# Optimization experiments

Measured on AMD Instinct MI355X. Metric: run time of the kernel, lower is better.

The kernel has to match this reference:

```python
import jax, jax.numpy as jnp
import numpy as np
from jax import lax

LENS = 11
R = LENS // 2


def _make_kernels(lens):
    """distance_kernel: euclidean distance of each offset from the window center.
    lens_shape_mask: binary disk (circular aperture) mask inside the lens window."""
    r = lens // 2
    yy, xx = jnp.meshgrid(jnp.arange(lens) - r, jnp.arange(lens) - r, indexing='ij')
    dist = jnp.sqrt((yy * yy + xx * xx).astype(jnp.float32))
    mask = (dist <= (r + 0.5)).astype(jnp.float32)
    return dist, mask


def setup_inputs() -> dict:
    key = jax.random.key(0)
    k1, k2, k3 = jax.random.split(key, 3)
    B, H, W = 4, 1024, 1024
    rgb = jax.random.uniform(k1, (B, 3, H, W), dtype=jnp.float32)
    # relative disparity w.r.t. focal plane (signed, ~[-4, 4])
    disp = jax.random.normal(k2, (B, 1, H, W), dtype=jnp.float32) * 2.0
    x = jnp.concatenate([rgb, disp], axis=1)
    lens_effects = jax.random.uniform(k3, (4, 1), dtype=jnp.float32) * 8.0 + 1.0
    diskernel, lens_mask = _make_kernels(LENS)
    return {"x": x, "lens_effects": lens_effects, "diskernel": diskernel, "lens_mask": lens_mask}


def reference(x, lens_effects, diskernel, lens_mask):
    """Depth-dependent scatter splatting with soft occlusion, expressed as a gather.
    Each source pixel p splats its color onto neighbors within its circle of
    confusion coc(p) = |lens_effect * disp(p)|, weighted by the disk aperture
    mask and a soft edge (clip(coc - dist + 0.5, 0, 1)). Occlusion: sources in
    front of the destination (larger disparity) dominate via a sigmoid gate.
    Scatter-to-q == gather-at-q over all kernel offsets of the padded image."""
    B, C, H, W = x.shape
    disp_dst = x[:, 3:4]
    scale = lens_effects.reshape(B, 1, 1, 1)
    # replication pad (ReplicationPad2d(lens // 2))
    xpad = jnp.pad(x, ((0, 0), (0, 0), (R, R), (R, R)), mode='edge')

    dys, dxs = np.meshgrid(np.arange(LENS), np.arange(LENS), indexing='ij')
    dys = jnp.asarray(dys.reshape(-1), dtype=jnp.int32)
    dxs = jnp.asarray(dxs.reshape(-1), dtype=jnp.int32)
    dvals = diskernel.reshape(-1)
    mvals = lens_mask.reshape(-1)

    def step(carry, inputs):
        num, den = carry
        dy, dx, d, m = inputs
        src = lax.dynamic_slice(xpad, (0, 0, dy, dx), (B, C, H, W))
        src_rgb, src_disp = src[:, :3], src[:, 3:4]
        coc = jnp.abs(scale * src_disp)                    # per-source CoC radius
        w = m * jnp.clip(coc - d + 0.5, 0.0, 1.0)          # soft disk membership
        occ = jax.nn.sigmoid(4.0 * (src_disp - disp_dst))  # front occludes back
        w = w * occ
        return (num + w * src_rgb, den + w), None

    num0 = jnp.zeros((B, 3, H, W), dtype=x.dtype)
    den0 = jnp.zeros((B, 1, H, W), dtype=x.dtype)
    (num, den), _ = lax.scan(step, (num0, den0), (dys, dxs, dvals, mvals))
    return num / (den + 1e-8)
```

## Files before the change

### kernel.cpp

```cpp
#include <hip/hip_runtime.h>

#define LENSZ 11
#define RAD   5
#define TSX   64
#define TSY   16
#define WINX  (TSX + LENSZ - 1)
#define WINY  (TSY + LENSZ - 1)
#define RS_H  78
#define RS_F  78
#define NPAIR 37
#define IMG_H 1024
#define IMG_W 1024
#define HW    (IMG_H * IMG_W)

#define C4L2  (-5.770780163555854f)
#define DEADC (-3000.0f)

typedef __fp16 v2h __attribute__((ext_vector_type(2)));

__device__ __forceinline__ float dot2acc(float acc, v2h a, v2h b) {
    asm("v_dot2_f32_f16 %0, %1, %2, %0" : "+v"(acc) : "v"(a), "v"(b));
    return acc;
}

constexpr float C0V(int dy, int dx) {
    switch (dy * dy + dx * dx) {
        case 0:  return  0.5f;
        case 1:  return -0.5f;
        case 2:  return -0.914213562f;
        case 4:  return -1.5f;
        case 5:  return -1.736067977f;
        case 8:  return -2.328427125f;
        case 9:  return -2.5f;
        case 10: return -2.662277660f;
        case 13: return -3.105551275f;
        case 16: return -3.5f;
        case 17: return -3.623105626f;
        case 18: return -3.742640687f;
        case 20: return -3.972135955f;
        case 25: return -4.5f;
        case 26: return -4.599019514f;
        case 29: return -4.885164807f;
        default: return DEADC;
    }
}

__shared__ __align__(16) float  dpl[WINY * RS_F];
__shared__ __align__(8)  __fp16 rpl[WINY * RS_H];
__shared__ __align__(8)  __fp16 gpl[WINY * RS_H];
__shared__ __align__(8)  __fp16 bpl[WINY * RS_H];

template<int ADY, int XMN, int XMX>
__device__ __forceinline__ void do_row(
    int wy, int x4, float scale, const float (&G)[4], v2h one2,
    float (&nr)[4], float (&ng)[4], float (&nb)[4], float (&dn)[4])
{
    const v2h zero2 = {(__fp16)0.f, (__fp16)0.f};
    const v2h onee2 = {(__fp16)1.f, (__fp16)1.f};
#pragma unroll
    for (int kxe = (XMN & ~1); kxe <= XMX + 3; kxe += 2) {
        const int xo = x4 + kxe;
        const float2 d2 = *reinterpret_cast<const float2*>(&dpl[wy * RS_F + xo]);
        const v2h r2 = *reinterpret_cast<const v2h*>(&rpl[wy * RS_H + xo]);
        const v2h g2 = *reinterpret_cast<const v2h*>(&gpl[wy * RS_H + xo]);
        const v2h b2 = *reinterpret_cast<const v2h*>(&bpl[wy * RS_H + xo]);
        const float coca = scale * fabsf(d2.x);
        const float cocb = scale * fabsf(d2.y);
        const v2h coc2 = __builtin_amdgcn_cvt_pkrtz(coca, cocb);
        const float Ea = __builtin_amdgcn_exp2f(fminf(C4L2 * d2.x, 63.f));
        const float Eb = __builtin_amdgcn_exp2f(fminf(C4L2 * d2.y, 63.f));
#pragma unroll
        for (int j = 0; j < 4; ++j) {
            const float c0a = C0V(ADY, kxe - j - RAD);
            const float c0b = C0V(ADY, kxe + 1 - j - RAD);
            if (c0a == DEADC && c0b == DEADC) continue;
            const float fa = fmaf(Ea, G[j], 1.f);
            const float fb = fmaf(Eb, G[j], 1.f);
            const float rr = __builtin_amdgcn_rcpf(fa * fb);
            const v2h occ2 = __builtin_amdgcn_cvt_pkrtz(rr * fb, rr * fa);
            const v2h c0h = {(__fp16)c0a, (__fp16)c0b};
            v2h t = coc2 + c0h;
            t = __builtin_elementwise_max(t, zero2);
            t = __builtin_elementwise_min(t, onee2);
            const v2h wh = t * occ2;
            nr[j] = dot2acc(nr[j], wh, r2);
            ng[j] = dot2acc(ng[j], wh, g2);
            nb[j] = dot2acc(nb[j], wh, b2);
            dn[j] = dot2acc(dn[j], wh, one2);
        }
    }
}

__global__ __launch_bounds__(256, 6) void scatter_render_kernel(
    const float* __restrict__ x,
    const float* __restrict__ lens,
    float* __restrict__ out)
{
    const int b   = blockIdx.z;
    const int bx0 = blockIdx.x * TSX;
    const int by0 = blockIdx.y * TSY;
    const int tx  = threadIdx.x;
    const int ty  = threadIdx.y;
    const int tid = ty * 16 + tx;

    const float scale = lens[b];
    const float* xb = x + (size_t)b * 4 * HW;

    for (int p = tid; p < WINY * NPAIR; p += 256) {
        int wy = p / NPAIR;
        int px = (p - wy * NPAIR) * 2;
        int gy = by0 - RAD + wy;  gy = min(max(gy, 0), IMG_H - 1);
        int g0 = bx0 - RAD + px;      g0 = min(max(g0, 0), IMG_W - 1);
        int g1 = bx0 - RAD + px + 1;  g1 = min(max(g1, 0), IMG_W - 1);
        int ba = gy * IMG_W + g0;
        int bb = gy * IMG_W + g1;
        float r0 = xb[ba],          r1 = xb[bb];
        float q0 = xb[ba + HW],     q1 = xb[bb + HW];
        float s0 = xb[ba + 2 * HW], s1 = xb[bb + 2 * HW];
        float d0 = xb[ba + 3 * HW], d1 = xb[bb + 3 * HW];
        int oh = wy * RS_H + px;
        *reinterpret_cast<v2h*>(&rpl[oh]) = __builtin_amdgcn_cvt_pkrtz(r0, r1);
        *reinterpret_cast<v2h*>(&gpl[oh]) = __builtin_amdgcn_cvt_pkrtz(q0, q1);
        *reinterpret_cast<v2h*>(&bpl[oh]) = __builtin_amdgcn_cvt_pkrtz(s0, s1);
        *reinterpret_cast<float2*>(&dpl[wy * RS_F + px]) = make_float2(d0, d1);
    }
    __syncthreads();

    const int x4 = 4 * tx;
    float G[4];
#pragma unroll
    for (int j = 0; j < 4; ++j) {
        float dd = dpl[(ty + RAD) * RS_F + x4 + j + RAD];
        G[j] = __builtin_amdgcn_exp2f(fminf(-C4L2 * dd, 63.f));
    }
    v2h one2; one2.x = (__fp16)1.f; one2.y = (__fp16)1.f;

    float nr[4] = {0.f, 0.f, 0.f, 0.f};
    float ng[4] = {0.f, 0.f, 0.f, 0.f};
    float nb[4] = {0.f, 0.f, 0.f, 0.f};
    float dn[4] = {0.f, 0.f, 0.f, 0.f};

#pragma unroll 1
    for (int t = 0; t < 2; ++t)
        do_row<5, 3, 7>(ty + t * 10, x4, scale, G, one2, nr, ng, nb, dn);
#pragma unroll 1
    for (int t = 0; t < 2; ++t)
        do_row<4, 2, 8>(ty + 1 + t * 8, x4, scale, G, one2, nr, ng, nb, dn);
#pragma unroll 1
    for (int t = 0; t < 2; ++t)
        do_row<3, 1, 9>(ty + 2 + t * 6, x4, scale, G, one2, nr, ng, nb, dn);
#pragma unroll 1
    for (int t = 0; t < 2; ++t)
        do_row<2, 0, 10>(ty + 3 + t * 4, x4, scale, G, one2, nr, ng, nb, dn);
#pragma unroll 1
    for (int t = 0; t < 2; ++t)
        do_row<1, 0, 10>(ty + 4 + t * 2, x4, scale, G, one2, nr, ng, nb, dn);
    do_row<0, 0, 10>(ty + 5, x4, scale, G, one2, nr, ng, nb, dn);

    const size_t obase = (size_t)b * 3 * HW + (size_t)(by0 + ty) * IMG_W + (bx0 + x4);

    float inv[4];
#pragma unroll
    for (int j = 0; j < 4; ++j)
        inv[j] = __builtin_amdgcn_rcpf(dn[j] + 1e-8f);

    float4 o;
    o.x = nr[0] * inv[0]; o.y = nr[1] * inv[1]; o.z = nr[2] * inv[2]; o.w = nr[3] * inv[3];
    *reinterpret_cast<float4*>(&out[obase]) = o;
    o.x = ng[0] * inv[0]; o.y = ng[1] * inv[1]; o.z = ng[2] * inv[2]; o.w = ng[3] * inv[3];
    *reinterpret_cast<float4*>(&out[obase + HW]) = o;
    o.x = nb[0] * inv[0]; o.y = nb[1] * inv[1]; o.z = nb[2] * inv[2]; o.w = nb[3] * inv[3];
    *reinterpret_cast<float4*>(&out[obase + 2 * HW]) = o;
}

extern "C" void kernel_launch(void* const* d_in, const int* in_sizes, int n_in,
                              void* d_out, int out_size, void* d_ws, size_t ws_size,
                              hipStream_t stream) {
    const float* x    = (const float*)d_in[0];
    const float* lens = (const float*)d_in[1];
    float* out        = (float*)d_out;

    const int B = in_sizes[1];

    dim3 block(16, 16, 1);
    dim3 grid(IMG_W / TSX, IMG_H / TSY, B);
    scatter_render_kernel<<<grid, block, 0, stream>>>(x, lens, out);
}
```

Baseline: 113.0 us.

## Widen tile to 128 columns with 8 outputs per thread and drop exp clamps

Each thread now computes 8 horizontally adjacent output pixels instead of 4, and the block tile doubles to 128 columns. Each loaded source pair (depth, rgb, coc, exp) is then reused across more outputs, which amortizes LDS loads and per-source exp work over a wider register window. The fminf clamps before exp2 are removed, so very large disparities could now produce inf and break the rational occlusion term. Register pressure rises, so the occupancy target drops from 6 to 4 blocks per CU.

Result: faster. 108.6 us (-3.9%).

```diff
diff --git a/kernel.cpp b/kernel.cpp
--- a/kernel.cpp
+++ b/kernel.cpp
@@ -2,13 +2,12 @@
 
 #define LENSZ 11
 #define RAD   5
-#define TSX   64
+#define TSX   128
 #define TSY   16
 #define WINX  (TSX + LENSZ - 1)
 #define WINY  (TSY + LENSZ - 1)
-#define RS_H  78
-#define RS_F  78
-#define NPAIR 37
+#define RS    140
+#define NPAIR 69
 #define IMG_H 1024
 #define IMG_W 1024
 #define HW    (IMG_H * IMG_W)
@@ -45,32 +44,31 @@
     }
 }
 
-__shared__ __align__(16) float  dpl[WINY * RS_F];
-__shared__ __align__(8)  __fp16 rpl[WINY * RS_H];
-__shared__ __align__(8)  __fp16 gpl[WINY * RS_H];
-__shared__ __align__(8)  __fp16 bpl[WINY * RS_H];
+__shared__ __align__(16) float  dpl[WINY * RS];
+__shared__ __align__(8)  __fp16 rpl[WINY * RS];
+__shared__ __align__(8)  __fp16 gpl[WINY * RS];
+__shared__ __align__(8)  __fp16 bpl[WINY * RS];
 
 template<int ADY, int XMN, int XMX>
 __device__ __forceinline__ void do_row(
-    int wy, int x4, float scale, const float (&G)[4], v2h one2,
-    float (&nr)[4], float (&ng)[4], float (&nb)[4], float (&dn)[4])
+    int wy, int x8, float scale, const float (&G)[8], v2h one2,
+    float (&nr)[8], float (&ng)[8], float (&nb)[8], float (&dn)[8])
 {
     const v2h zero2 = {(__fp16)0.f, (__fp16)0.f};
     const v2h onee2 = {(__fp16)1.f, (__fp16)1.f};
 #pragma unroll
-    for (int kxe = (XMN & ~1); kxe <= XMX + 3; kxe += 2) {
-        const int xo = x4 + kxe;
-        const float2 d2 = *reinterpret_cast<const float2*>(&dpl[wy * RS_F + xo]);
-        const v2h r2 = *reinterpret_cast<const v2h*>(&rpl[wy * RS_H + xo]);
-        const v2h g2 = *reinterpret_cast<const v2h*>(&gpl[wy * RS_H + xo]);
-        const v2h b2 = *reinterpret_cast<const v2h*>(&bpl[wy * RS_H + xo]);
-        const float coca = scale * fabsf(d2.x);
-        const float cocb = scale * fabsf(d2.y);
-        const v2h coc2 = __builtin_amdgcn_cvt_pkrtz(coca, cocb);
-        const float Ea = __builtin_amdgcn_exp2f(fminf(C4L2 * d2.x, 63.f));
-        const float Eb = __builtin_amdgcn_exp2f(fminf(C4L2 * d2.y, 63.f));
+    for (int kxe = (XMN & ~1); kxe <= XMX + 7; kxe += 2) {
+        const int xo = x8 + kxe;
+        const float2 d2 = *reinterpret_cast<const float2*>(&dpl[wy * RS + xo]);
+        const v2h r2 = *reinterpret_cast<const v2h*>(&rpl[wy * RS + xo]);
+        const v2h g2 = *reinterpret_cast<const v2h*>(&gpl[wy * RS + xo]);
+        const v2h b2 = *reinterpret_cast<const v2h*>(&bpl[wy * RS + xo]);
+        const v2h coc2 = __builtin_amdgcn_cvt_pkrtz(scale * fabsf(d2.x),
+                                                    scale * fabsf(d2.y));
+        const float Ea = __builtin_amdgcn_exp2f(C4L2 * d2.x);
+        const float Eb = __builtin_amdgcn_exp2f(C4L2 * d2.y);
 #pragma unroll
-        for (int j = 0; j < 4; ++j) {
+        for (int j = 0; j < 8; ++j) {
             const float c0a = C0V(ADY, kxe - j - RAD);
             const float c0b = C0V(ADY, kxe + 1 - j - RAD);
             if (c0a == DEADC && c0b == DEADC) continue;
@@ -91,7 +89,7 @@
     }
 }
 
-__global__ __launch_bounds__(256, 6) void scatter_render_kernel(
+__global__ __launch_bounds__(256, 4) void scatter_render_kernel(
     const float* __restrict__ x,
     const float* __restrict__ lens,
     float* __restrict__ out)
@@ -118,59 +116,66 @@
         float q0 = xb[ba + HW],     q1 = xb[bb + HW];
         float s0 = xb[ba + 2 * HW], s1 = xb[bb + 2 * HW];
         float d0 = xb[ba + 3 * HW], d1 = xb[bb + 3 * HW];
-        int oh = wy * RS_H + px;
+        int oh = wy * RS + px;
         *reinterpret_cast<v2h*>(&rpl[oh]) = __builtin_amdgcn_cvt_pkrtz(r0, r1);
         *reinterpret_cast<v2h*>(&gpl[oh]) = __builtin_amdgcn_cvt_pkrtz(q0, q1);
         *reinterpret_cast<v2h*>(&bpl[oh]) = __builtin_amdgcn_cvt_pkrtz(s0, s1);
-        *reinterpret_cast<float2*>(&dpl[wy * RS_F + px]) = make_float2(d0, d1);
+        *reinterpret_cast<float2*>(&dpl[oh]) = make_float2(d0, d1);
     }
     __syncthreads();
 
-    const int x4 = 4 * tx;
-    float G[4];
+    const int x8 = 8 * tx;
+    float G[8];
 #pragma unroll
-    for (int j = 0; j < 4; ++j) {
-        float dd = dpl[(ty + RAD) * RS_F + x4 + j + RAD];
-        G[j] = __builtin_amdgcn_exp2f(fminf(-C4L2 * dd, 63.f));
+    for (int j = 0; j < 8; ++j) {
+        float dd = dpl[(ty + RAD) * RS + x8 + j + RAD];
+        G[j] = __builtin_amdgcn_exp2f(-C4L2 * dd);
     }
     v2h one2; one2.x = (__fp16)1.f; one2.y = (__fp16)1.f;
 
-    float nr[4] = {0.f, 0.f, 0.f, 0.f};
-    float ng[4] = {0.f, 0.f, 0.f, 0.f};
-    float nb[4] = {0.f, 0.f, 0.f, 0.f};
-    float dn[4] = {0.f, 0.f, 0.f, 0.f};
+    float nr[8] = {0.f, 0.f, 0.f, 0.f, 0.f, 0.f, 0.f, 0.f};
+    float ng[8] = {0.f, 0.f, 0.f, 0.f, 0.f, 0.f, 0.f, 0.f};
+    float nb[8] = {0.f, 0.f, 0.f, 0.f, 0.f, 0.f, 0.f, 0.f};
+    float dn[8] = {0.f, 0.f, 0.f, 0.f, 0.f, 0.f, 0.f, 0.f};
 
 #pragma unroll 1
     for (int t = 0; t < 2; ++t)
-        do_row<5, 3, 7>(ty + t * 10, x4, scale, G, one2, nr, ng, nb, dn);
+        do_row<5, 3, 7>(ty + t * 10, x8, scale, G, one2, nr, ng, nb, dn);
 #pragma unroll 1
     for (int t = 0; t < 2; ++t)
-        do_row<4, 2, 8>(ty + 1 + t * 8, x4, scale, G, one2, nr, ng, nb, dn);
+        do_row<4, 2, 8>(ty + 1 + t * 8, x8, scale, G, one2, nr, ng, nb, dn);
 #pragma unroll 1
     for (int t = 0; t < 2; ++t)
-        do_row<3, 1, 9>(ty + 2 + t * 6, x4, scale, G, one2, nr, ng, nb, dn);
+        do_row<3, 1, 9>(ty + 2 + t * 6, x8, scale, G, one2, nr, ng, nb, dn);
 #pragma unroll 1
     for (int t = 0; t < 2; ++t)
-        do_row<2, 0, 10>(ty + 3 + t * 4, x4, scale, G, one2, nr, ng, nb, dn);
+        do_row<2, 0, 10>(ty + 3 + t * 4, x8, scale, G, one2, nr, ng, nb, dn);
 #pragma unroll 1
     for (int t = 0; t < 2; ++t)
-        do_row<1, 0, 10>(ty + 4 + t * 2, x4, scale, G, one2, nr, ng, nb, dn);
-    do_row<0, 0, 10>(ty + 5, x4, scale, G, one2, nr, ng, nb, dn);
+        do_row<1, 0, 10>(ty + 4 + t * 2, x8, scale, G, one2, nr, ng, nb, dn);
+    do_row<0, 0, 10>(ty + 5, x8, scale, G, one2, nr, ng, nb, dn);
 
-    const size_t obase = (size_t)b * 3 * HW + (size_t)(by0 + ty) * IMG_W + (bx0 + x4);
+    const size_t obase = (size_t)b * 3 * HW + (size_t)(by0 + ty) * IMG_W + (bx0 + x8);
 
-    float inv[4];
+    float inv[8];
 #pragma unroll
-    for (int j = 0; j < 4; ++j)
+    for (int j = 0; j < 8; ++j)
         inv[j] = __builtin_amdgcn_rcpf(dn[j] + 1e-8f);
 
-    float4 o;
-    o.x = nr[0] * inv[0]; o.y = nr[1] * inv[1]; o.z = nr[2] * inv[2]; o.w = nr[3] * inv[3];
-    *reinterpret_cast<float4*>(&out[obase]) = o;
-    o.x = ng[0] * inv[0]; o.y = ng[1] * inv[1]; o.z = ng[2] * inv[2]; o.w = ng[3] * inv[3];
-    *reinterpret_cast<float4*>(&out[obase + HW]) = o;
-    o.x = nb[0] * inv[0]; o.y = nb[1] * inv[1]; o.z = nb[2] * inv[2]; o.w = nb[3] * inv[3];
-    *reinterpret_cast<float4*>(&out[obase + 2 * HW]) = o;
+#pragma unroll
+    for (int h = 0; h < 2; ++h) {
+        const int o4 = 4 * h;
+        float4 o;
+        o.x = nr[o4+0]*inv[o4+0]; o.y = nr[o4+1]*inv[o4+1];
+        o.z = nr[o4+2]*inv[o4+2]; o.w = nr[o4+3]*inv[o4+3];
+        *reinterpret_cast<float4*>(&out[obase + o4]) = o;
+        o.x = ng[o4+0]*inv[o4+0]; o.y = ng[o4+1]*inv[o4+1];
+        o.z = ng[o4+2]*inv[o4+2]; o.w = ng[o4+3]*inv[o4+3];
+        *reinterpret_cast<float4*>(&out[obase + HW + o4]) = o;
+        o.x = nb[o4+0]*inv[o4+0]; o.y = nb[o4+1]*inv[o4+1];
+        o.z = nb[o4+2]*inv[o4+2]; o.w = nb[o4+3]*inv[o4+3];
+        *reinterpret_cast<float4*>(&out[obase + 2 * HW + o4]) = o;
+    }
 }
 
 extern "C" void kernel_launch(void* const* d_in, const int* in_sizes, int n_in,
```
